# Optimization experiments

Measured on AMD Instinct MI355X. Metric: run time of the kernel, lower is better.

The kernel has to match this reference:

```python
import jax, jax.numpy as jnp
import numpy as np

T, B, H, L = 512, 64, 100, 10  # seq_len, batch, hidden, num_layers


def setup_inputs() -> dict:
    key = jax.random.key(0)
    ks = jax.random.split(key, 8)
    s = 0.1  # ~ PyTorch uniform(-1/sqrt(H), 1/sqrt(H)) scale
    return {
        "x": jax.random.normal(ks[0], (T, B, H), jnp.float32),
        "W_ih0": jax.random.normal(ks[1], (2, H, H), jnp.float32) * s,
        "W_ih": jax.random.normal(ks[2], (L - 1, 2, H, 2 * H), jnp.float32) * s,
        "W_hh": jax.random.normal(ks[3], (L, 2, H, H), jnp.float32) * s,
        "b_ih": jax.random.normal(ks[4], (L, 2, H), jnp.float32) * s,
        "b_hh": jax.random.normal(ks[5], (L, 2, H), jnp.float32) * s,
        "W_out": jax.random.normal(ks[6], (1, 2 * H), jnp.float32) * s,
        "b_out": jax.random.normal(ks[7], (1,), jnp.float32) * s,
    }


def _rnn_dir(x, Wih, Whh, b, reverse):
    # Precompute input projection for all timesteps as one big GEMM.
    # z: [T, B, H]; b already holds b_ih + b_hh.
    z = jnp.einsum('tbi,hi->tbh', x, Wih) + b
    h0 = jnp.zeros((x.shape[1], Whh.shape[0]), x.dtype)

    def step(h, zt):
        h = jnp.tanh(zt + h @ Whh.T)
        return h, h

    # reverse=True scans backward in time but emits outputs in original order,
    # exactly matching the backward direction of a bidirectional RNN.
    _, ys = jax.lax.scan(step, h0, z, reverse=reverse)
    return ys  # [T, B, H]


def reference(x, W_ih0, W_ih, W_hh, b_ih, b_hh, W_out, b_out):
    h = x
    for l in range(L):
        Wih_l = W_ih0 if l == 0 else W_ih[l - 1]
        fwd = _rnn_dir(h, Wih_l[0], W_hh[l, 0], b_ih[l, 0] + b_hh[l, 0], False)
        bwd = _rnn_dir(h, Wih_l[1], W_hh[l, 1], b_ih[l, 1] + b_hh[l, 1], True)
        h = jnp.concatenate([fwd, bwd], axis=-1)  # [T, B, 2H]
    y = jax.nn.sigmoid(jnp.einsum('tbh,oh->tbo', h, W_out) + b_out)  # [T, B, 1]
    return y.reshape(-1)  # [T*B]
```

## Files before the change

kernel.cpp:

```cpp
#include <hip/hip_runtime.h>
#include <math.h>


#define T_LEN 512
#define BATCH 64
#define HID   100
#define M_TOT (T_LEN * BATCH)
#define KPAD  224
#define NPAD  208
#define WPLANE (NPAD * KPAD)

typedef unsigned short ushort_t;
typedef unsigned int   uint_t;
typedef __attribute__((ext_vector_type(8))) __bf16 bf16x8;
typedef __attribute__((ext_vector_type(4))) float f32x4;
typedef __attribute__((ext_vector_type(8))) unsigned int uintx8;

__global__ __launch_bounds__(256) void ingemm_kernel(
    const float* __restrict__ In, const float* __restrict__ W,
    const float* __restrict__ bih, const float* __restrict__ bhh,
    float* __restrict__ z, int K)
{
    __shared__ float As[16][132];
    __shared__ float Bs[16][68];
    const int tid = threadIdx.x;
    const int m0 = blockIdx.x * 128;
    const int n0 = blockIdx.y * 64;
    const int tx = tid & 15, ty = tid >> 4;
    const int lm = tid >> 2;
    const int lk = (tid & 3) << 2;

    float acc[8][4];
    #pragma unroll
    for (int i = 0; i < 8; ++i)
        #pragma unroll
        for (int j = 0; j < 4; ++j) acc[i][j] = 0.f;

    for (int k0 = 0; k0 < K; k0 += 16) {
        #pragma unroll
        for (int rep = 0; rep < 2; ++rep) {
            float4 av = make_float4(0.f,0.f,0.f,0.f);
            const int row = lm + 64 * rep;
            if (k0 + lk < K)
                av = *(const float4*)(In + (size_t)(m0 + row) * K + k0 + lk);
            As[lk+0][row]=av.x; As[lk+1][row]=av.y;
            As[lk+2][row]=av.z; As[lk+3][row]=av.w;
        }
        {
            float4 bv = make_float4(0.f,0.f,0.f,0.f);
            const int nrow = n0 + lm;
            if (nrow < 200 && k0 + lk < K)
                bv = *(const float4*)(W + (size_t)nrow * K + k0 + lk);
            Bs[lk+0][lm]=bv.x; Bs[lk+1][lm]=bv.y;
            Bs[lk+2][lm]=bv.z; Bs[lk+3][lm]=bv.w;
        }
        __syncthreads();
        #pragma unroll
        for (int kk = 0; kk < 16; ++kk) {
            float4 alo = *(const float4*)&As[kk][ty << 2];
            float4 ahi = *(const float4*)&As[kk][64 + (ty << 2)];
            float4 b4  = *(const float4*)&Bs[kk][tx << 2];
            float a[8] = {alo.x, alo.y, alo.z, alo.w,
                          ahi.x, ahi.y, ahi.z, ahi.w};
            float b[4] = {b4.x, b4.y, b4.z, b4.w};
            #pragma unroll
            for (int i = 0; i < 8; ++i)
                #pragma unroll
                for (int j = 0; j < 4; ++j)
                    acc[i][j] += a[i] * b[j];
        }
        __syncthreads();
    }
    #pragma unroll
    for (int i = 0; i < 8; ++i) {
        const int m = m0 + ((i < 4) ? ((ty << 2) + i) : (64 + (ty << 2) + (i - 4)));
        #pragma unroll
        for (int j = 0; j < 4; ++j) {
            const int n = n0 + (tx << 2) + j;
            if (n < 200) {
                const int dir = (n >= 100) ? 1 : 0;
                const int h = n - dir * 100;
                z[(size_t)dir * M_TOT * HID + (size_t)m * HID + h] =
                    acc[i][j] + bih[n] + bhh[n];
            }
        }
    }
}

__device__ __forceinline__ unsigned bf16_rne(float v) {
    unsigned u = __float_as_uint(v);
    return (u + 0x7FFFu + ((u >> 16) & 1u)) >> 16;
}

__global__ __launch_bounds__(256) void zeropad_kernel(uint_t* a, uint_t* b)
{
    int i = blockIdx.x * 256 + threadIdx.x;
    if (i >= M_TOT * 24) return;
    size_t off = (size_t)(i / 24) * KPAD + 200 + (i % 24);
    a[off] = 0; b[off] = 0;
}

__global__ __launch_bounds__(256) void wsplit_all_kernel(
    const float* __restrict__ W_ih, ushort_t* __restrict__ wbuf)
{
    int i = blockIdx.x * 256 + threadIdx.x;
    if (i >= 9 * WPLANE) return;
    int l = i / WPLANE;
    int r = i - l * WPLANE;
    int n = r / KPAD, k = r - (r / KPAD) * KPAD;
    const float* W = W_ih + (size_t)l * 2 * 100 * 200;
    float v = (n < 200 && k < 200) ? W[n * 200 + k] : 0.f;
    unsigned hr = bf16_rne(v);
    float hv = __uint_as_float(hr << 16);
    unsigned lr = bf16_rne(v - hv);
    ushort_t* whi = wbuf + (size_t)l * 2 * WPLANE;
    whi[r] = (ushort_t)hr;
    whi[WPLANE + r] = (ushort_t)lr;
}

__global__ __launch_bounds__(256) void ingemm_mfma_kernel(
    const uint_t* __restrict__ in_pk,
    const ushort_t* __restrict__ w_hi,  const ushort_t* __restrict__ w_lo,
    const float* __restrict__ bih, const float* __restrict__ bhh,
    float* __restrict__ z)
{
    const int wv   = threadIdx.x >> 6;
    const int lane = threadIdx.x & 63;
    const int mt   = blockIdx.x * 4 + wv;
    const int m0   = mt * 16;
    const int r16  = lane & 15;
    const int kg   = lane >> 4;
    const int kof  = kg * 8;

    bf16x8 ah[7], al[7];
    const uint_t* arp = in_pk + (size_t)(m0 + r16) * KPAD + kof;
    #pragma unroll
    for (int c = 0; c < 7; ++c) {
        uintx8 p = *(const uintx8*)(arp + 32 * c);
        union { bf16x8 v; ushort_t u[8]; } hh, ll;
        #pragma unroll
        for (int i = 0; i < 8; ++i) {
            hh.u[i] = (ushort_t)(p[i] & 0xFFFFu);
            ll.u[i] = (ushort_t)(p[i] >> 16);
        }
        ah[c] = hh.v; al[c] = ll.v;
    }

    for (int nt = 0; nt < 13; ++nt) {
        const int n0 = nt * 16;
        const ushort_t* brh = w_hi + (size_t)(n0 + r16) * KPAD + kof;
        const ushort_t* brl = w_lo + (size_t)(n0 + r16) * KPAD + kof;
        f32x4 acc = {0.f, 0.f, 0.f, 0.f};
        #pragma unroll
        for (int c = 0; c < 7; ++c) {
            bf16x8 bh = *(const bf16x8*)(brh + 32 * c);
            bf16x8 bl = *(const bf16x8*)(brl + 32 * c);
            acc = __builtin_amdgcn_mfma_f32_16x16x32_bf16(ah[c], bh, acc, 0, 0, 0);
            acc = __builtin_amdgcn_mfma_f32_16x16x32_bf16(ah[c], bl, acc, 0, 0, 0);
            acc = __builtin_amdgcn_mfma_f32_16x16x32_bf16(al[c], bh, acc, 0, 0, 0);
        }
        const int n = n0 + r16;
        if (n < 200) {
            const int dir = (n >= 100) ? 1 : 0;
            const int h = n - dir * 100;
            const float bias = bih[n] + bhh[n];
            #pragma unroll
            for (int r = 0; r < 4; ++r) {
                const int m = m0 + kg * 4 + r;
                z[(size_t)dir * M_TOT * HID + (size_t)m * HID + h] = acc[r] + bias;
            }
        }
    }
}

__device__ __forceinline__ float dpp_qxor1(float x) {
    int i = __float_as_int(x);
    i = __builtin_amdgcn_update_dpp(0, i, 0xB1, 0xF, 0xF, false);
    return __int_as_float(i);
}
__device__ __forceinline__ float dpp_qxor2(float x) {
    int i = __float_as_int(x);
    i = __builtin_amdgcn_update_dpp(0, i, 0x4E, 0xF, 0xF, false);
    return __int_as_float(i);
}
__device__ __forceinline__ float dpp_hmir(float x) {
    int i = __float_as_int(x);
    i = __builtin_amdgcn_update_dpp(0, i, 0x141, 0xF, 0xF, false);
    return __int_as_float(i);
}

__global__ __launch_bounds__(256) void scan_kernel(
    const float* __restrict__ z,
    const float* __restrict__ Whh,
    uint_t* __restrict__ opk)
{
    const int dir = blockIdx.x >> 6;
    const int b   = blockIdx.x & 63;
    const int tid = threadIdx.x;
    const int w   = tid >> 6;
    const int lane= tid & 63;
    const int q   = lane & 3;
    const int b2  = (lane >> 2) & 1;
    const int ks  = q | (b2 << 2);
    const int slot= (lane >> 3) + 8 * w;
    const bool active = (slot < 25);
    const int slotc = active ? slot : 24;
    const int jout = 4 * slotc + q;
    const bool writer = active && (b2 == 0);
    const int kb = 12 * ks;

    __shared__ float h_lds[2][112];
    for (int i = tid; i < 224; i += 256) (&h_lds[0][0])[i] = 0.f;

    float w4[4][16];
    #pragma unroll
    for (int r = 0; r < 4; ++r) {
        const float* wr = Whh + ((size_t)dir * HID + 4 * slotc + r) * HID + kb;
        #pragma unroll
        for (int i = 0; i < 4; ++i) {
            float4 v = *(const float4*)(wr + 4 * i);
            w4[r][4*i+0] = v.x; w4[r][4*i+1] = v.y;
            w4[r][4*i+2] = v.z; w4[r][4*i+3] = v.w;
        }
        if (ks > 0) {
            w4[r][0] = 0.f; w4[r][1] = 0.f; w4[r][2] = 0.f; w4[r][3] = 0.f;
        }
    }
    __syncthreads();

    const ptrdiff_t zstride = BATCH * HID;
    const ptrdiff_t ostride = BATCH * KPAD;
    const int t0 = dir ? (T_LEN - 1) : 0;
    const ptrdiff_t zstep = dir ? -zstride : zstride;
    const ptrdiff_t ostep = dir ? -ostride : ostride;
    const ptrdiff_t zstep2 = 2 * zstep, zstep3 = 3 * zstep, zstep4 = 4 * zstep;

    const float* zp = z + (size_t)dir * M_TOT * HID + (size_t)b * HID + jout
                        + (ptrdiff_t)t0 * zstride;
    uint_t* op = opk + ((size_t)t0 * BATCH + b) * KPAD + dir * HID + jout;

    float zr0 = zp[0];
    float zr1 = zp[zstep];
    float zr2 = zp[zstep2];
    float zr3 = zp[zstep3];
    const float* zpf = zp + zstep4;

#define RNN_STEP(ZREG, DO_PF, PFOFF, RD, WRB)                           \
  do {                                                                  \
    const float zin = ZREG;                                             \
    if (DO_PF) ZREG = *(zpf + (PFOFF));                                 \
    const float4* hp = (const float4*)((RD) + kb);                      \
    float a0 = 0.f, a1 = 0.f, a2 = 0.f, a3 = 0.f;                       \
    _Pragma("unroll")                                                   \
    for (int i = 0; i < 4; ++i) {                                       \
      float4 hv = hp[i];                                                \
      a0 += w4[0][4*i+0] * hv.x; a0 += w4[0][4*i+1] * hv.y;             \
      a0 += w4[0][4*i+2] * hv.z; a0 += w4[0][4*i+3] * hv.w;             \
      a1 += w4[1][4*i+0] * hv.x; a1 += w4[1][4*i+1] * hv.y;             \
      a1 += w4[1][4*i+2] * hv.z; a1 += w4[1][4*i+3] * hv.w;             \
      a2 += w4[2][4*i+0] * hv.x; a2 += w4[2][4*i+1] * hv.y;             \
      a2 += w4[2][4*i+2] * hv.z; a2 += w4[2][4*i+3] * hv.w;             \
      a3 += w4[3][4*i+0] * hv.x; a3 += w4[3][4*i+1] * hv.y;             \
      a3 += w4[3][4*i+2] * hv.z; a3 += w4[3][4*i+3] * hv.w;             \
    }                                                                   \
    float t0_ = a0 + dpp_hmir(a0);                                      \
    float t1_ = a1 + dpp_hmir(a1);                                      \
    float t2_ = a2 + dpp_hmir(a2);                                      \
    float t3_ = a3 + dpp_hmir(a3);                                      \
    float k01 = (q & 1) ? t1_ : t0_;                                    \
    float s01s = (q & 1) ? t0_ : t1_;                                   \
    float s01 = k01 + dpp_qxor1(s01s);                                  \
    float k23 = (q & 1) ? t3_ : t2_;                                    \
    float s23s = (q & 1) ? t2_ : t3_;                                   \
    float s23 = k23 + dpp_qxor1(s23s);                                  \
    float kf = (q & 2) ? s23 : s01;                                     \
    float sf = (q & 2) ? s01 : s23;                                     \
    float tot = kf + dpp_qxor2(sf);                                     \
    float xin = zin + tot;                                              \
    float ax = fabsf(xin);                                              \
    float e = __expf(2.f * ax);                                         \
    float r = 1.f - 2.f / (e + 1.f);                                    \
    float val = copysignf(r, xin);                                      \
    if (writer) {                                                       \
      (WRB)[jout] = val;                                                \
      unsigned hr = bf16_rne(val);                                      \
      float hv2 = __uint_as_float(hr << 16);                            \
      unsigned lr = bf16_rne(val - hv2);                                \
      *op = hr | (lr << 16);                                            \
    }                                                                   \
    op += ostep;                                                        \
    asm volatile("s_waitcnt lgkmcnt(0)" ::: "memory");                  \
    __builtin_amdgcn_sched_barrier(0);                                  \
    __builtin_amdgcn_s_barrier();                                       \
    __builtin_amdgcn_sched_barrier(0);                                  \
  } while (0)

    float* const h0 = &h_lds[0][0];
    float* const h1 = &h_lds[1][0];

    for (int g = 0; g < (T_LEN / 4) - 1; ++g) {
        RNN_STEP(zr0, 1, 0,      h0, h1);
        RNN_STEP(zr1, 1, zstep,  h1, h0);
        RNN_STEP(zr2, 1, zstep2, h0, h1);
        RNN_STEP(zr3, 1, zstep3, h1, h0);
        zpf += zstep4;
    }
    RNN_STEP(zr0, 0, 0, h0, h1);
    RNN_STEP(zr1, 0, 0, h1, h0);
    RNN_STEP(zr2, 0, 0, h0, h1);
    RNN_STEP(zr3, 0, 0, h1, h0);

#undef RNN_STEP
}

__global__ __launch_bounds__(256) void outproj_kernel(
    const uint_t* __restrict__ hpk,
    const float* __restrict__ Wout, const float* __restrict__ bout,
    float* __restrict__ y)
{
    const int gid = blockIdx.x * 256 + threadIdx.x;
    const int wid = gid >> 6;
    const int lane = threadIdx.x & 63;
    if (wid >= M_TOT) return;
    const uint_t* rp = hpk + (size_t)wid * KPAD;
    float acc = 0.f;
    for (int k = lane; k < 200; k += 64) {
        uint_t p = rp[k];
        float hv = __uint_as_float(p << 16)
                 + __uint_as_float(p & 0xFFFF0000u);
        acc += hv * Wout[k];
    }
    #pragma unroll
    for (int off = 32; off > 0; off >>= 1) acc += __shfl_xor(acc, off);
    if (lane == 0) y[wid] = 1.f / (1.f + __expf(-(acc + bout[0])));
}

extern "C" void kernel_launch(void* const* d_in, const int* in_sizes, int n_in,
                              void* d_out, int out_size, void* d_ws, size_t ws_size,
                              hipStream_t stream)
{
    const float* x     = (const float*)d_in[0];
    const float* W_ih0 = (const float*)d_in[1];
    const float* W_ih  = (const float*)d_in[2];
    const float* W_hh  = (const float*)d_in[3];
    const float* b_ih  = (const float*)d_in[4];
    const float* b_hh  = (const float*)d_in[5];
    const float* W_out = (const float*)d_in[6];
    const float* b_out = (const float*)d_in[7];
    float* y = (float*)d_out;

    float* z = (float*)d_ws;
    uint_t* pkA = (uint_t*)(z + (size_t)2 * M_TOT * HID);
    uint_t* pkB = pkA + (size_t)M_TOT * KPAD;
    ushort_t* wbuf = (ushort_t*)(pkB + (size_t)M_TOT * KPAD);

    zeropad_kernel<<<(M_TOT * 24 + 255) / 256, 256, 0, stream>>>(pkA, pkB);
    wsplit_all_kernel<<<(9 * WPLANE + 255) / 256, 256, 0, stream>>>(W_ih, wbuf);

    ingemm_kernel<<<dim3(M_TOT / 128, 4), 256, 0, stream>>>(
        x, W_ih0, b_ih, b_hh, z, 100);
    scan_kernel<<<128, 256, 0, stream>>>(z, W_hh, pkA);

    for (int l = 1; l < 10; ++l) {
        const uint_t* in = (l & 1) ? pkA : pkB;
        uint_t* out      = (l & 1) ? pkB : pkA;
        const ushort_t* whi = wbuf + (size_t)(l - 1) * 2 * WPLANE;
        ingemm_mfma_kernel<<<512, 256, 0, stream>>>(
            in, whi, whi + WPLANE, b_ih + l * 200, b_hh + l * 200, z);
        scan_kernel<<<128, 256, 0, stream>>>(
            z, W_hh + (size_t)l * 2 * HID * HID, out);
    }
    outproj_kernel<<<M_TOT / 4, 256, 0, stream>>>(pkB, W_out, b_out, y);
}
```

Baseline: 2.070 ms.

## Use split-bf16 MFMA for layer-0 input GEMM and defer packed output store

Replaces the fp32 SIMT GEMM for layer 0 with the templated split-bf16 MFMA GEMM. It adds kernels that pack x and W_ih0 into hi/lo bf16 planes padded to K=128, staging packed x in pkB before the zero-pad pass. In the scan step, the packed global store moves after the barrier and uses a cheaper truncating hi split, taking it off the critical path before synchronisation. This adds two small preprocessing kernels, and the truncated hi part slightly changes rounding.

```diff
diff --git a/kernel.cpp b/kernel.cpp
--- a/kernel.cpp
+++ b/kernel.cpp
@@ -7,8 +7,10 @@
 #define HID   100
 #define M_TOT (T_LEN * BATCH)
 #define KPAD  224
+#define KP0   128
 #define NPAD  208
 #define WPLANE (NPAD * KPAD)
+#define W0PLANE (NPAD * KP0)
 
 typedef unsigned short ushort_t;
 typedef unsigned int   uint_t;
@@ -16,80 +18,14 @@
 typedef __attribute__((ext_vector_type(4))) float f32x4;
 typedef __attribute__((ext_vector_type(8))) unsigned int uintx8;
 
-__global__ __launch_bounds__(256) void ingemm_kernel(
-    const float* __restrict__ In, const float* __restrict__ W,
-    const float* __restrict__ bih, const float* __restrict__ bhh,
-    float* __restrict__ z, int K)
-{
-    __shared__ float As[16][132];
-    __shared__ float Bs[16][68];
-    const int tid = threadIdx.x;
-    const int m0 = blockIdx.x * 128;
-    const int n0 = blockIdx.y * 64;
-    const int tx = tid & 15, ty = tid >> 4;
-    const int lm = tid >> 2;
-    const int lk = (tid & 3) << 2;
-
-    float acc[8][4];
-    #pragma unroll
-    for (int i = 0; i < 8; ++i)
-        #pragma unroll
-        for (int j = 0; j < 4; ++j) acc[i][j] = 0.f;
-
-    for (int k0 = 0; k0 < K; k0 += 16) {
-        #pragma unroll
-        for (int rep = 0; rep < 2; ++rep) {
-            float4 av = make_float4(0.f,0.f,0.f,0.f);
-            const int row = lm + 64 * rep;
-            if (k0 + lk < K)
-                av = *(const float4*)(In + (size_t)(m0 + row) * K + k0 + lk);
-            As[lk+0][row]=av.x; As[lk+1][row]=av.y;
-            As[lk+2][row]=av.z; As[lk+3][row]=av.w;
-        }
-        {
-            float4 bv = make_float4(0.f,0.f,0.f,0.f);
-            const int nrow = n0 + lm;
-            if (nrow < 200 && k0 + lk < K)
-                bv = *(const float4*)(W + (size_t)nrow * K + k0 + lk);
-            Bs[lk+0][lm]=bv.x; Bs[lk+1][lm]=bv.y;
-            Bs[lk+2][lm]=bv.z; Bs[lk+3][lm]=bv.w;
-        }
-        __syncthreads();
-        #pragma unroll
-        for (int kk = 0; kk < 16; ++kk) {
-            float4 alo = *(const float4*)&As[kk][ty << 2];
-            float4 ahi = *(const float4*)&As[kk][64 + (ty << 2)];
-            float4 b4  = *(const float4*)&Bs[kk][tx << 2];
-            float a[8] = {alo.x, alo.y, alo.z, alo.w,
-                          ahi.x, ahi.y, ahi.z, ahi.w};
-            float b[4] = {b4.x, b4.y, b4.z, b4.w};
-            #pragma unroll
-            for (int i = 0; i < 8; ++i)
-                #pragma unroll
-                for (int j = 0; j < 4; ++j)
-                    acc[i][j] += a[i] * b[j];
-        }
-        __syncthreads();
-    }
-    #pragma unroll
-    for (int i = 0; i < 8; ++i) {
-        const int m = m0 + ((i < 4) ? ((ty << 2) + i) : (64 + (ty << 2) + (i - 4)));
-        #pragma unroll
-        for (int j = 0; j < 4; ++j) {
-            const int n = n0 + (tx << 2) + j;
-            if (n < 200) {
-                const int dir = (n >= 100) ? 1 : 0;
-                const int h = n - dir * 100;
-                z[(size_t)dir * M_TOT * HID + (size_t)m * HID + h] =
-                    acc[i][j] + bih[n] + bhh[n];
-            }
-        }
-    }
-}
-
 __device__ __forceinline__ unsigned bf16_rne(float v) {
     unsigned u = __float_as_uint(v);
     return (u + 0x7FFFu + ((u >> 16) & 1u)) >> 16;
+}
+__device__ __forceinline__ uint_t pack_hilo(float v) {
+    unsigned u = __float_as_uint(v);
+    float lo = v - __uint_as_float(u & 0xFFFF0000u);
+    return (u >> 16) | (bf16_rne(lo) << 16);
 }
 
 __global__ __launch_bounds__(256) void zeropad_kernel(uint_t* a, uint_t* b)
@@ -118,6 +54,31 @@
     whi[WPLANE + r] = (ushort_t)lr;
 }
 
+__global__ __launch_bounds__(256) void wsplit0_kernel(
+    const float* __restrict__ W_ih0, ushort_t* __restrict__ w0buf)
+{
+    int i = blockIdx.x * 256 + threadIdx.x;
+    if (i >= W0PLANE) return;
+    int n = i >> 7, k = i & 127;
+    float v = (n < 200 && k < 100) ? W_ih0[n * 100 + k] : 0.f;
+    unsigned hr = bf16_rne(v);
+    float hv = __uint_as_float(hr << 16);
+    unsigned lr = bf16_rne(v - hv);
+    w0buf[i] = (ushort_t)hr;
+    w0buf[W0PLANE + i] = (ushort_t)lr;
+}
+
+__global__ __launch_bounds__(256) void xsplit_kernel(
+    const float* __restrict__ x, uint_t* __restrict__ xpk)
+{
+    int i = blockIdx.x * 256 + threadIdx.x;
+    if (i >= M_TOT * KP0) return;
+    int m = i >> 7, k = i & 127;
+    float v = (k < 100) ? x[(size_t)m * 100 + k] : 0.f;
+    xpk[i] = pack_hilo(v);
+}
+
+template<int NC, int KP>
 __global__ __launch_bounds__(256) void ingemm_mfma_kernel(
     const uint_t* __restrict__ in_pk,
     const ushort_t* __restrict__ w_hi,  const ushort_t* __restrict__ w_lo,
@@ -132,10 +93,10 @@
     const int kg   = lane >> 4;
     const int kof  = kg * 8;
 
-    bf16x8 ah[7], al[7];
-    const uint_t* arp = in_pk + (size_t)(m0 + r16) * KPAD + kof;
+    bf16x8 ah[NC], al[NC];
+    const uint_t* arp = in_pk + (size_t)(m0 + r16) * KP + kof;
     #pragma unroll
-    for (int c = 0; c < 7; ++c) {
+    for (int c = 0; c < NC; ++c) {
         uintx8 p = *(const uintx8*)(arp + 32 * c);
         union { bf16x8 v; ushort_t u[8]; } hh, ll;
         #pragma unroll
@@ -148,11 +109,11 @@
 
     for (int nt = 0; nt < 13; ++nt) {
         const int n0 = nt * 16;
-        const ushort_t* brh = w_hi + (size_t)(n0 + r16) * KPAD + kof;
-        const ushort_t* brl = w_lo + (size_t)(n0 + r16) * KPAD + kof;
+        const ushort_t* brh = w_hi + (size_t)(n0 + r16) * KP + kof;
+        const ushort_t* brl = w_lo + (size_t)(n0 + r16) * KP + kof;
         f32x4 acc = {0.f, 0.f, 0.f, 0.f};
         #pragma unroll
-        for (int c = 0; c < 7; ++c) {
+        for (int c = 0; c < NC; ++c) {
             bf16x8 bh = *(const bf16x8*)(brh + 32 * c);
             bf16x8 bl = *(const bf16x8*)(brl + 32 * c);
             acc = __builtin_amdgcn_mfma_f32_16x16x32_bf16(ah[c], bh, acc, 0, 0, 0);
@@ -281,18 +242,13 @@
     float e = __expf(2.f * ax);                                         \
     float r = 1.f - 2.f / (e + 1.f);                                    \
     float val = copysignf(r, xin);                                      \
-    if (writer) {                                                       \
-      (WRB)[jout] = val;                                                \
-      unsigned hr = bf16_rne(val);                                      \
-      float hv2 = __uint_as_float(hr << 16);                            \
-      unsigned lr = bf16_rne(val - hv2);                                \
-      *op = hr | (lr << 16);                                            \
-    }                                                                   \
-    op += ostep;                                                        \
+    if (writer) (WRB)[jout] = val;                                      \
     asm volatile("s_waitcnt lgkmcnt(0)" ::: "memory");                  \
     __builtin_amdgcn_sched_barrier(0);                                  \
     __builtin_amdgcn_s_barrier();                                       \
     __builtin_amdgcn_sched_barrier(0);                                  \
+    if (writer) *op = pack_hilo(val);          \
+    op += ostep;                                                        \
   } while (0)
 
     float* const h0 = &h_lds[0][0];
@@ -353,19 +309,23 @@
     uint_t* pkA = (uint_t*)(z + (size_t)2 * M_TOT * HID);
     uint_t* pkB = pkA + (size_t)M_TOT * KPAD;
     ushort_t* wbuf = (ushort_t*)(pkB + (size_t)M_TOT * KPAD);
-
+    ushort_t* w0buf = wbuf + (size_t)9 * 2 * WPLANE;
+    uint_t* xpk = pkB;
+
+    wsplit_all_kernel<<<(9 * WPLANE + 255) / 256, 256, 0, stream>>>(W_ih, wbuf);
+    wsplit0_kernel<<<(W0PLANE + 255) / 256, 256, 0, stream>>>(W_ih0, w0buf);
+    xsplit_kernel<<<(M_TOT * KP0) / 256, 256, 0, stream>>>(x, xpk);
+
+    ingemm_mfma_kernel<4, KP0><<<512, 256, 0, stream>>>(
+        xpk, w0buf, w0buf + W0PLANE, b_ih, b_hh, z);
     zeropad_kernel<<<(M_TOT * 24 + 255) / 256, 256, 0, stream>>>(pkA, pkB);
-    wsplit_all_kernel<<<(9 * WPLANE + 255) / 256, 256, 0, stream>>>(W_ih, wbuf);
-
-    ingemm_kernel<<<dim3(M_TOT / 128, 4), 256, 0, stream>>>(
-        x, W_ih0, b_ih, b_hh, z, 100);
     scan_kernel<<<128, 256, 0, stream>>>(z, W_hh, pkA);
 
     for (int l = 1; l < 10; ++l) {
         const uint_t* in = (l & 1) ? pkA : pkB;
         uint_t* out      = (l & 1) ? pkB : pkA;
         const ushort_t* whi = wbuf + (size_t)(l - 1) * 2 * WPLANE;
-        ingemm_mfma_kernel<<<512, 256, 0, stream>>>(
+        ingemm_mfma_kernel<7, KPAD><<<512, 256, 0, stream>>>(
             in, whi, whi + WPLANE, b_ih + l * 200, b_hh + l * 200, z);
         scan_kernel<<<128, 256, 0, stream>>>(
             z, W_hh + (size_t)l * 2 * HID * HID, out);
```

New measurement: 2.142 ms. +3.5%, slower.
